# Kernel tuning notes

Measured on AMD Instinct MI355X. Metric: run time of the kernel, lower is better.

The kernel has to match this reference:

```python
import jax, jax.numpy as jnp
import numpy as np

B, L, HID, H, DH = 1, 2048, 1024, 16, 64
KW = 2  # d_conv
EPS = float(np.finfo(np.float32).eps)  # torch RMSNorm eps=None -> dtype eps


def _causal_dw_conv(x, w, b):
    # x: (B, L, D), w: (D, K), b: (D,). Depthwise causal conv, no activation.
    Bs, Ls, D = x.shape
    K = w.shape[1]
    xp = jnp.pad(x, ((0, 0), (K - 1, 0), (0, 0)))
    out = b
    for k in range(K):
        out = out + xp[:, k:k + Ls, :] * w[:, k]
    return out


def setup_inputs() -> dict:
    key = jax.random.key(0)
    ks = jax.random.split(key, 14)
    hidden_states = jax.random.normal(ks[0], (B, L, HID), jnp.float32)
    # masked_fill(attention_mask != 0, -inf): True above diagonal (future masked)
    attention_mask = jnp.triu(jnp.ones((L, L), dtype=bool), 1)[None, None]
    all_dim = 3 * H * DH  # q_size + 2*kv_size with KVH == H
    qkv_w = jax.random.normal(ks[1], (all_dim, HID), jnp.float32) * 0.02
    q_conv_w = jax.random.normal(ks[2], (H * DH, KW), jnp.float32) * 0.5
    q_conv_b = jax.random.normal(ks[3], (H * DH,), jnp.float32) * 0.02
    k_conv_w = jax.random.normal(ks[4], (H * DH, KW), jnp.float32) * 0.5
    k_conv_b = jax.random.normal(ks[5], (H * DH,), jnp.float32) * 0.02
    v_conv_w = jax.random.normal(ks[6], (H * DH, KW), jnp.float32) * 0.5
    v_conv_b = jax.random.normal(ks[7], (H * DH,), jnp.float32) * 0.02
    norm_w = jnp.ones((DH,), jnp.float32)
    A_log = jnp.log(jax.random.uniform(ks[8], (H,), jnp.float32, 1.0, 16.0))
    dt0 = jnp.exp(jax.random.uniform(ks[9], (H,), jnp.float32)
                  * (np.log(0.1) - np.log(0.001)) + np.log(0.001))
    dt0 = jnp.clip(dt0, 1e-4)
    dt_bias = dt0 + jnp.log(-jnp.expm1(-dt0))  # inverse softplus init
    dt_proj_w = jax.random.normal(ks[10], (H, HID), jnp.float32) * 0.02
    dt_proj_b = jnp.zeros((H,), jnp.float32)
    o_w = jax.random.normal(ks[11], (HID, H * DH), jnp.float32) * 0.02
    order_coeff = jnp.ones((1, H, 1, 1), jnp.float32)  # 1/cumprod(arange(1,2))
    return dict(hidden_states=hidden_states, attention_mask=attention_mask,
                qkv_w=qkv_w, q_conv_w=q_conv_w, q_conv_b=q_conv_b,
                k_conv_w=k_conv_w, k_conv_b=k_conv_b, v_conv_w=v_conv_w,
                v_conv_b=v_conv_b, norm_w=norm_w, A_log=A_log, dt_bias=dt_bias,
                dt_proj_w=dt_proj_w, dt_proj_b=dt_proj_b, o_w=o_w,
                order_coeff=order_coeff)


def reference(hidden_states, attention_mask, qkv_w, q_conv_w, q_conv_b,
              k_conv_w, k_conv_b, v_conv_w, v_conv_b, norm_w, A_log, dt_bias,
              dt_proj_w, dt_proj_b, o_w, order_coeff):
    qs = H * DH
    qkv = hidden_states @ qkv_w.T                    # (B, L, 3*H*DH)
    q = _causal_dw_conv(qkv[..., :qs], q_conv_w, q_conv_b)
    k = _causal_dw_conv(qkv[..., qs:2 * qs], k_conv_w, k_conv_b)
    v = _causal_dw_conv(qkv[..., 2 * qs:], v_conv_w, v_conv_b)
    # split heads -> (B, H, L, DH)
    q = q.reshape(B, L, H, DH).transpose(0, 2, 1, 3)
    k = k.reshape(B, L, H, DH).transpose(0, 2, 1, 3)
    v = v.reshape(B, L, H, DH).transpose(0, 2, 1, 3)
    # SSM-style gate: dt (B, L, H)
    dt = jax.nn.softplus(hidden_states @ dt_proj_w.T + dt_proj_b + dt_bias)
    v = v * jnp.swapaxes(dt, 1, 2)[..., None]        # value scaled by dt
    A = -jnp.exp(A_log)[None, None, :] * dt          # (B, L, H)
    A_cumsum = jnp.swapaxes(jnp.cumsum(A, axis=1), 1, 2)  # (B, H, L)
    diff = A_cumsum[:, :, :, None] - A_cumsum[:, :, None, :]  # (B, H, L, L)
    A_mask = jnp.exp(jnp.where(attention_mask, -jnp.inf, diff))
    # order == 1: Taylor series reduces to a single gated linear term
    scores = jnp.einsum('bhld,bhmd->bhlm', q, k) * A_mask * (1.0 / order_coeff)
    out = scores @ v                                  # (B, H, L, DH)
    # RMSNorm over head_dim
    out = out * jax.lax.rsqrt(jnp.mean(out * out, -1, keepdims=True) + EPS) * norm_w
    out = out.transpose(0, 2, 1, 3).reshape(B, L, H * DH)
    return out @ o_w.T
```

## Files before the change

### kernel.cpp

```cpp
#include <hip/hip_runtime.h>
#include <hip/hip_bf16.h>

#define L_SEQ 2048
#define HIDN  1024
#define NH    16
#define DHD   64
#define QKV_P 3200
#define QC_S  2048
#define LP    72

typedef float f4 __attribute__((ext_vector_type(4)));
typedef __bf16 bf16x8 __attribute__((ext_vector_type(8)));
typedef _Float16 half8 __attribute__((ext_vector_type(8)));

union H8 {
  half8 h;
  uint4 u4;
};

__device__ __forceinline__ float b2f(unsigned short u) {
  union { unsigned int i; float f; } c; c.i = ((unsigned int)u) << 16; return c.f;
}
__device__ __forceinline__ unsigned short f2b(float f) {
  union { float f; unsigned int i; } c; c.f = f;
  unsigned int r = c.i + 0x7FFFu + ((c.i >> 16) & 1u);
  return (unsigned short)(r >> 16);
}
__device__ __forceinline__ unsigned short f2h(float f) {
  union { _Float16 h; unsigned short u; } c; c.h = (_Float16)f; return c.u;
}

__global__ __launch_bounds__(256) void prep_kernel(
    const void* hs, const void* qkvw, const void* ow, const void* dtw,
    const void* qw, const void* qb, const void* kw, const void* kb,
    const void* vw, const void* vb, const void* nw, const void* al,
    const void* dtb, const void* dpb, const void* oc,
    unsigned short* __restrict__ hs_b, unsigned short* __restrict__ qkvw_b,
    unsigned short* __restrict__ ow_b,
    float* __restrict__ smallf, int* __restrict__ flag)
{
  __shared__ int cnt;
  if (threadIdx.x == 0) cnt = 0;
  __syncthreads();
  {
    const unsigned short* p = (const unsigned short*)hs;
    int c = 0;
    for (int i = threadIdx.x; i < 8192; i += 256)
      if (((p[i] >> 7) & 0xFFu) >= 140u) c++;
    atomicAdd(&cnt, c);
  }
  __syncthreads();
  const int f = (cnt >= 32) ? 1 : 0;
  if (blockIdx.x == 0 && threadIdx.x == 0) *flag = f;

  const int tid = blockIdx.x * 256 + threadIdx.x;
  const int nth = gridDim.x * 256;
  for (int i = tid; i < 1605632; i += nth) {
    const void* src; unsigned short* dst; int off;
    if (i < 524288)       { src = hs;   dst = hs_b;   off = i; }
    else if (i < 1310720) { src = qkvw; dst = qkvw_b; off = i - 524288; }
    else if (i < 1314816) { src = dtw;  dst = qkvw_b + 3072 * 1024; off = i - 1310720; }
    else if (i < 1343488) {
      *(ushort4*)(qkvw_b + 3088 * 1024 + (i - 1314816) * 4) = (ushort4){0, 0, 0, 0};
      continue;
    }
    else                  { src = ow;   dst = ow_b;   off = i - 1343488; }
    const int e = off * 4;
    if (f) {
      f4 v = *(const f4*)((const float*)src + e);
      ushort4 o;
      o.x = f2b(v[0]); o.y = f2b(v[1]); o.z = f2b(v[2]); o.w = f2b(v[3]);
      *(ushort4*)(dst + e) = o;
    } else {
      *(uint2*)(dst + e) = *(const uint2*)((const unsigned short*)src + e);
    }
  }
  const void* ptrs[11] = {qw, qb, kw, kb, vw, vb, nw, al, dtb, dpb, oc};
  const int sizes[11] = {2048, 1024, 2048, 1024, 2048, 1024, 64, 16, 16, 16, 16};
  int off = 0;
  for (int a = 0; a < 11; ++a) {
    for (int i = tid; i < sizes[a]; i += nth)
      smallf[off + i] = f ? ((const float*)ptrs[a])[i]
                          : b2f(((const unsigned short*)ptrs[a])[i]);
    off += sizes[a];
  }
}

__global__ __launch_bounds__(256) void gemm128(
    const unsigned short* __restrict__ A, const unsigned short* __restrict__ B,
    float* __restrict__ C, int M, int N, int K)
{
  __shared__ __align__(16) unsigned short As[128 * 40];
  __shared__ __align__(16) unsigned short Bs[128 * 40];
  const int t = threadIdx.x;
  const int w = t >> 6, lane = t & 63;
  const int quad = lane >> 4, l16 = lane & 15;
  const int wr = w >> 1, wc = w & 1;
  const int m0 = blockIdx.y * 128, n0 = blockIdx.x * 128;
  const int srow = t >> 1;
  const int scol = (t & 1) * 16;

  f4 acc[4][4];
#pragma unroll
  for (int i = 0; i < 4; ++i)
#pragma unroll
    for (int j = 0; j < 4; ++j) acc[i][j] = (f4){0.f, 0.f, 0.f, 0.f};

  const unsigned short* apg = A + (size_t)(m0 + srow) * K + scol;
  const unsigned short* bpg = B + (size_t)(n0 + srow) * K + scol;
  uint4 a0 = *(const uint4*)apg,       a1 = *(const uint4*)(apg + 8);
  uint4 b0 = *(const uint4*)bpg,       b1 = *(const uint4*)(bpg + 8);

  for (int k0 = 0; k0 < K; k0 += 32) {
    __syncthreads();
    *(uint4*)&As[srow * 40 + scol]     = a0;
    *(uint4*)&As[srow * 40 + scol + 8] = a1;
    *(uint4*)&Bs[srow * 40 + scol]     = b0;
    *(uint4*)&Bs[srow * 40 + scol + 8] = b1;
    __syncthreads();
    if (k0 + 32 < K) {
      a0 = *(const uint4*)(apg + k0 + 32); a1 = *(const uint4*)(apg + k0 + 40);
      b0 = *(const uint4*)(bpg + k0 + 32); b1 = *(const uint4*)(bpg + k0 + 40);
    }
    bf16x8 aF[4], bF[4];
#pragma unroll
    for (int i = 0; i < 4; ++i)
      aF[i] = *(const bf16x8*)&As[(wr * 64 + i * 16 + l16) * 40 + quad * 8];
#pragma unroll
    for (int j = 0; j < 4; ++j)
      bF[j] = *(const bf16x8*)&Bs[(wc * 64 + j * 16 + l16) * 40 + quad * 8];
#pragma unroll
    for (int i = 0; i < 4; ++i)
#pragma unroll
      for (int j = 0; j < 4; ++j)
        acc[i][j] = __builtin_amdgcn_mfma_f32_16x16x32_bf16(aF[i], bF[j], acc[i][j], 0, 0, 0);
  }

#pragma unroll
  for (int i = 0; i < 4; ++i)
#pragma unroll
    for (int j = 0; j < 4; ++j)
#pragma unroll
      for (int r = 0; r < 4; ++r) {
        int m = m0 + wr * 64 + i * 16 + quad * 4 + r;
        int n = n0 + wc * 64 + j * 16 + l16;
        C[(size_t)m * N + n] = acc[i][j][r];
      }
}

template <int MODE>
__global__ __launch_bounds__(256) void gemm_bt(
    const unsigned short* __restrict__ A, const unsigned short* __restrict__ B,
    void* __restrict__ Cv, int M, int N, int K, const int* __restrict__ flag)
{
  __shared__ __align__(16) short As[64 * 40];
  __shared__ __align__(16) short Bs[64 * 40];
  const int t = threadIdx.x;
  const int wave = t >> 6, lane = t & 63;
  const int quad = lane >> 4, l16 = lane & 15;
  const int m0 = blockIdx.y * 64, n0 = blockIdx.x * 64;
  const int srow = t >> 2, scol = (t & 3) * 8;
  f4 acc[4];
#pragma unroll
  for (int i = 0; i < 4; ++i) acc[i] = (f4){0.f, 0.f, 0.f, 0.f};
  const unsigned short* ap = A + (size_t)(m0 + srow) * K + scol;
  const unsigned short* bp = B + (size_t)(n0 + srow) * K + scol;
  for (int k0 = 0; k0 < K; k0 += 32) {
    uint4 av = *(const uint4*)(ap + k0);
    uint4 bv = *(const uint4*)(bp + k0);
    __syncthreads();
    *(uint4*)&As[srow * 40 + scol] = av;
    *(uint4*)&Bs[srow * 40 + scol] = bv;
    __syncthreads();
    bf16x8 af = *(const bf16x8*)&As[(wave * 16 + l16) * 40 + quad * 8];
#pragma unroll
    for (int nt = 0; nt < 4; ++nt) {
      bf16x8 bf = *(const bf16x8*)&Bs[(nt * 16 + l16) * 40 + quad * 8];
      acc[nt] = __builtin_amdgcn_mfma_f32_16x16x32_bf16(af, bf, acc[nt], 0, 0, 0);
    }
  }
  const int outf32 = (MODE == 0) ? 1 : (*flag ? 1 : 0);
#pragma unroll
  for (int nt = 0; nt < 4; ++nt) {
#pragma unroll
    for (int r = 0; r < 4; ++r) {
      int m = m0 + wave * 16 + quad * 4 + r;
      int n = n0 + nt * 16 + l16;
      if (outf32) ((float*)Cv)[(size_t)m * N + n] = acc[nt][r];
      else        ((unsigned short*)Cv)[(size_t)m * N + n] = f2b(acc[nt][r]);
    }
  }
}

__global__ __launch_bounds__(256) void conv_kernel(
    const float* __restrict__ qkvf, const float* __restrict__ smallf,
    unsigned short* __restrict__ qc, unsigned short* __restrict__ vt,
    float* __restrict__ Ac)
{
  if (blockIdx.x < 4096) {
    const int idx = blockIdx.x * 256 + threadIdx.x;
    const int l = idx >> 9;
    const int c = (idx & 511) * 4;
    f4 xc = *(const f4*)&qkvf[(size_t)l * QKV_P + c];
    f4 xp = (f4){0.f, 0.f, 0.f, 0.f};
    if (l > 0) xp = *(const f4*)&qkvf[(size_t)(l - 1) * QKV_P + c];
    const float* w; const float* b; int cb;
    if (c < HIDN) { w = smallf;        b = smallf + 2048; cb = c; }
    else          { w = smallf + 3072; b = smallf + 5120; cb = c - HIDN; }
    f4 o;
#pragma unroll
    for (int j = 0; j < 4; ++j)
      o[j] = b[cb + j] + xp[j] * w[(cb + j) * 2] + xc[j] * w[(cb + j) * 2 + 1];
    ushort4 st;
    st.x = f2h(o[0]); st.y = f2h(o[1]); st.z = f2h(o[2]); st.w = f2h(o[3]);
    *(ushort4*)&qc[(size_t)l * QC_S + c] = st;
  } else if (blockIdx.x < 4608) {
    __shared__ __align__(16) unsigned short Ts[64 * 68];
    const int bv = blockIdx.x - 4096;
    const int h = bv & 15;
    const int lt0 = bv >> 4;
    const int t = threadIdx.x;
    const int srow = t >> 2, cc = t & 3;
    const int l = lt0 * 64 + srow;
    const int cb = h * 64 + cc * 16;
    const float* w = smallf + 6144;
    const float* b = smallf + 8192;
    const float z = qkvf[(size_t)l * QKV_P + 3072 + h]
                  + smallf[9312 + h] + smallf[9296 + h];
    const float dtv = (z > 20.f) ? z : log1pf(expf(z));
    const float* xcp = &qkvf[(size_t)l * QKV_P + 2048 + cb];
    const float* xpp = &qkvf[(size_t)(l - 1) * QKV_P + 2048 + cb];
    unsigned short o16[16];
#pragma unroll
    for (int g = 0; g < 4; ++g) {
      f4 xc = *(const f4*)(xcp + g * 4);
      f4 xp = (f4){0.f, 0.f, 0.f, 0.f};
      if (l > 0) xp = *(const f4*)(xpp + g * 4);
#pragma unroll
      for (int j = 0; j < 4; ++j) {
        const int ch = cb + g * 4 + j;
        float o = b[ch] + xp[j] * w[ch * 2] + xc[j] * w[ch * 2 + 1];
        o16[g * 4 + j] = f2h(o * dtv);
      }
    }
    *(uint4*)&Ts[srow * 68 + cc * 16]     = *(const uint4*)&o16[0];
    *(uint4*)&Ts[srow * 68 + cc * 16 + 8] = *(const uint4*)&o16[8];
    __syncthreads();
    __align__(16) unsigned short o[16];
#pragma unroll
    for (int j = 0; j < 16; ++j) o[j] = Ts[(cc * 16 + j) * 68 + srow];
    unsigned short* op = vt + ((size_t)h * DHD + srow) * L_SEQ + lt0 * 64 + cc * 16;
    *(uint4*)op = *(const uint4*)&o[0];
    *(uint4*)(op + 8) = *(const uint4*)&o[8];
  } else {
    const int h = blockIdx.x - 4608;
    const int lane = threadIdx.x;
    if (lane < 64) {
      const int base = lane * 32;
      const float dpb = smallf[9312 + h], dtb = smallf[9296 + h];
      const float nal = -expf(smallf[9280 + h]);
      float Av[32];
      float run = 0.f;
#pragma unroll
      for (int i = 0; i < 32; ++i) {
        const int l = base + i;
        float z = qkvf[(size_t)l * QKV_P + 3072 + h] + dpb + dtb;
        float dtv = (z > 20.f) ? z : log1pf(expf(z));
        Av[i] = nal * dtv;
        run += Av[i];
      }
      float incl = run;
#pragma unroll
      for (int off = 1; off < 64; off <<= 1) {
        float n = __shfl_up(incl, off);
        if (lane >= off) incl += n;
      }
      float r2 = incl - run;
#pragma unroll
      for (int i = 0; i < 32; ++i) {
        r2 += Av[i];
        Ac[h * L_SEQ + base + i] = r2;
      }
    }
  }
}

__global__ __launch_bounds__(256) void attn_kernel(
    const unsigned short* __restrict__ qc,
    const unsigned short* __restrict__ vt,
    const float* __restrict__ Ac,
    const float* __restrict__ smallf,
    float* __restrict__ po)
{
  const int n  = blockIdx.x;
  const int r_ = n & 7;
  const int hh = (n >> 3) & 1;
  const int k_ = n >> 4;
  const int h  = r_ + 8 * hh;
  const int lt = 31 - (k_ >> 1);
  const int s_ = k_ & 1;
  const int nT = lt + 1;
  const int mS = s_ ? ((nT + 1) >> 1) : 0;
  const int mE = s_ ? nT : ((nT + 1) >> 1);

  const int t  = threadIdx.x;
  const int w    = t >> 6;
  const int lane = t & 63;
  const int l16  = lane & 15;
  const int quad = lane >> 4;
  const int srow = t >> 2;
  const int cc   = t & 3;

  __shared__ __align__(16) unsigned short K_lds[2][64 * LP];
  __shared__ __align__(16) unsigned short V_lds[2][64 * LP];
  __shared__ __align__(16) unsigned short S_lds[64 * LP];

  const int l0 = lt * 64;
  const float rc = 1.0f / smallf[9328 + h];
  const float* Acp = Ac + h * L_SEQ;

  H8 qf0, qf1;
  {
    const unsigned short* qp =
        qc + (size_t)(l0 + w * 16 + l16) * QC_S + h * DHD + quad * 8;
    qf0.u4 = *(const uint4*)qp;
    qf1.u4 = *(const uint4*)(qp + 32);
  }
  float alv[4];
#pragma unroll
  for (int r = 0; r < 4; ++r) alv[r] = Acp[l0 + w * 16 + quad * 4 + r];

  f4 acc[4];
#pragma unroll
  for (int i = 0; i < 4; ++i) acc[i] = (f4){0.f, 0.f, 0.f, 0.f};

  const unsigned short* kgp =
      qc + (size_t)srow * QC_S + HIDN + h * DHD + cc * 16;
  const unsigned short* vgp =
      vt + ((size_t)h * DHD + srow) * L_SEQ + cc * 16;
  const int swo = srow * LP + cc * 16;

  if (mS < mE) {
    uint4 k0v = *(const uint4*)(kgp + (size_t)mS * 64 * QC_S);
    uint4 k1v = *(const uint4*)(kgp + (size_t)mS * 64 * QC_S + 8);
    uint4 v0v = *(const uint4*)(vgp + (size_t)mS * 64);
    uint4 v1v = *(const uint4*)(vgp + (size_t)mS * 64 + 8);
    float amv[4];
#pragma unroll
    for (int nt = 0; nt < 4; ++nt) amv[nt] = Acp[mS * 64 + nt * 16 + l16];

    *(uint4*)&K_lds[0][swo]     = k0v;
    *(uint4*)&K_lds[0][swo + 8] = k1v;
    *(uint4*)&V_lds[0][swo]     = v0v;
    *(uint4*)&V_lds[0][swo + 8] = v1v;
    __syncthreads();

    int cur = 0;
    for (int it = mS; it < mE; ++it) {
      uint4 nk0 = k0v, nk1 = k1v, nv0 = v0v, nv1 = v1v;
      float namv[4];
      const bool more = (it + 1 < mE);
      if (more) {
        const unsigned short* kp = kgp + (size_t)(it + 1) * 64 * QC_S;
        const unsigned short* vp = vgp + (size_t)(it + 1) * 64;
        nk0 = *(const uint4*)kp; nk1 = *(const uint4*)(kp + 8);
        nv0 = *(const uint4*)vp; nv1 = *(const uint4*)(vp + 8);
#pragma unroll
        for (int nt = 0; nt < 4; ++nt)
          namv[nt] = Acp[(it + 1) * 64 + nt * 16 + l16];
      }

      f4 s[4];
#pragma unroll
      for (int i = 0; i < 4; ++i) s[i] = (f4){0.f, 0.f, 0.f, 0.f};
#pragma unroll
      for (int ks = 0; ks < 2; ++ks) {
        H8 qk = ks ? qf1 : qf0;
#pragma unroll
        for (int nt = 0; nt < 4; ++nt) {
          H8 kf;
          kf.u4 = *(const uint4*)&K_lds[cur][(nt * 16 + l16) * LP + ks * 32 + quad * 8];
          s[nt] = __builtin_amdgcn_mfma_f32_16x16x32_f16(qk.h, kf.h, s[nt], 0, 0, 0);
        }
      }
      const int m0 = it * 64;
      if (it == lt) {
#pragma unroll
        for (int nt = 0; nt < 4; ++nt) {
          const int mg = m0 + nt * 16 + l16;
          const float am = amv[nt];
#pragma unroll
          for (int r = 0; r < 4; ++r) {
            const int lg = l0 + w * 16 + quad * 4 + r;
            float val = (mg <= lg) ? s[nt][r] * __expf(alv[r] - am) * rc : 0.0f;
            S_lds[(w * 16 + quad * 4 + r) * LP + nt * 16 + l16] = f2h(val);
          }
        }
      } else {
#pragma unroll
        for (int nt = 0; nt < 4; ++nt) {
          const float am = amv[nt];
#pragma unroll
          for (int r = 0; r < 4; ++r) {
            float val = s[nt][r] * __expf(alv[r] - am) * rc;
            S_lds[(w * 16 + quad * 4 + r) * LP + nt * 16 + l16] = f2h(val);
          }
        }
      }
#pragma unroll
      for (int ks = 0; ks < 2; ++ks) {
        H8 sa;
        sa.u4 = *(const uint4*)&S_lds[(w * 16 + l16) * LP + ks * 32 + quad * 8];
#pragma unroll
        for (int db = 0; db < 4; ++db) {
          H8 vb;
          vb.u4 = *(const uint4*)&V_lds[cur][(db * 16 + l16) * LP + ks * 32 + quad * 8];
          acc[db] = __builtin_amdgcn_mfma_f32_16x16x32_f16(sa.h, vb.h, acc[db], 0, 0, 0);
        }
      }
      if (more) {
        unsigned short* Kl = K_lds[cur ^ 1];
        unsigned short* Vl = V_lds[cur ^ 1];
        *(uint4*)&Kl[swo]     = nk0;
        *(uint4*)&Kl[swo + 8] = nk1;
        *(uint4*)&Vl[swo]     = nv0;
        *(uint4*)&Vl[swo + 8] = nv1;
#pragma unroll
        for (int nt = 0; nt < 4; ++nt) amv[nt] = namv[nt];
        __syncthreads();
        cur ^= 1;
      }
    }
  }

  float* pout = po + (size_t)s_ * (L_SEQ * HIDN);
#pragma unroll
  for (int r = 0; r < 4; ++r) {
    float* op = pout + (size_t)(l0 + w * 16 + quad * 4 + r) * HIDN + h * DHD + l16;
#pragma unroll
    for (int db = 0; db < 4; ++db)
      op[db * 16] = acc[db][r];
  }
}

__global__ __launch_bounds__(256) void reduce_kernel(
    const float* __restrict__ po, const float* __restrict__ smallf,
    unsigned short* __restrict__ attn_out)
{
  const int l = blockIdx.x;
  const int t = threadIdx.x;
  const int col = t * 4;
  const float* p0 = po + (size_t)l * HIDN + col;
  const float* p1 = p0 + (size_t)L_SEQ * HIDN;
  f4 a = *(const f4*)p0;
  f4 b = *(const f4*)p1;
  f4 o = a + b;
  float p = o[0] * o[0] + o[1] * o[1] + o[2] * o[2] + o[3] * o[3];
#pragma unroll
  for (int off = 1; off < 16; off <<= 1) p += __shfl_xor(p, off);
  const float rn = rsqrtf(p * (1.0f / 64.0f) + 1.1920928955078125e-07f);
  const int d0 = col & 63;
  ushort4 st;
  st.x = f2b(o[0] * rn * smallf[9216 + d0]);
  st.y = f2b(o[1] * rn * smallf[9216 + d0 + 1]);
  st.z = f2b(o[2] * rn * smallf[9216 + d0 + 2]);
  st.w = f2b(o[3] * rn * smallf[9216 + d0 + 3]);
  *(ushort4*)&attn_out[(size_t)l * HIDN + col] = st;
}

extern "C" void kernel_launch(void* const* d_in, const int* in_sizes, int n_in,
                              void* d_out, int out_size, void* d_ws, size_t ws_size,
                              hipStream_t stream)
{
  (void)in_sizes; (void)n_in; (void)out_size; (void)ws_size;
  const void* hs        = d_in[0];
  const void* qkv_w     = d_in[2];
  const void* q_conv_w  = d_in[3];
  const void* q_conv_b  = d_in[4];
  const void* k_conv_w  = d_in[5];
  const void* k_conv_b  = d_in[6];
  const void* v_conv_w  = d_in[7];
  const void* v_conv_b  = d_in[8];
  const void* norm_w    = d_in[9];
  const void* A_log     = d_in[10];
  const void* dt_bias   = d_in[11];
  const void* dt_proj_w = d_in[12];
  const void* dt_proj_b = d_in[13];
  const void* o_w       = d_in[14];
  const void* ordc      = d_in[15];

  char* ws = (char*)d_ws;
  int* flag             = (int*)ws;
  unsigned short* hs_b  = (unsigned short*)(ws + 256);
  unsigned short* qkvw_b= (unsigned short*)(ws + 4194560);
  unsigned short* ow_b  = (unsigned short*)(ws + 10748160);
  float* smallf         = (float*)(ws + 12845312);
  float* qkvf           = (float*)(ws + 12882688);
  unsigned short* qc_h  = (unsigned short*)(ws + 39097088);
  float* Acum           = (float*)(ws + 47616768);
  unsigned short* attnb = (unsigned short*)(ws + 47747840);
  unsigned short* vt_h  = (unsigned short*)(ws + 51942144);
  float* po             = (float*)(ws + 56136448);

  prep_kernel<<<1024, 256, 0, stream>>>(
      hs, qkv_w, o_w, dt_proj_w,
      q_conv_w, q_conv_b, k_conv_w, k_conv_b, v_conv_w, v_conv_b,
      norm_w, A_log, dt_bias, dt_proj_b, ordc,
      hs_b, qkvw_b, ow_b, smallf, flag);

  gemm128<<<dim3(QKV_P / 128, L_SEQ / 128), 256, 0, stream>>>(
      hs_b, qkvw_b, qkvf, L_SEQ, QKV_P, HIDN);
  conv_kernel<<<4096 + 512 + 16, 256, 0, stream>>>(qkvf, smallf, qc_h, vt_h, Acum);
  attn_kernel<<<1024, 256, 0, stream>>>(qc_h, vt_h, Acum, smallf, po);
  reduce_kernel<<<L_SEQ, 256, 0, stream>>>(po, smallf, attnb);
  gemm_bt<1><<<dim3(HIDN / 64, L_SEQ / 64), 256, 0, stream>>>(
      attnb, ow_b, d_out, L_SEQ, HIDN, HIDN, flag);
}
```

Baseline: 220.7 us.

## Load GEMM tiles directly into LDS and raise wave priority around MFMA blocks

The bf16 GEMM now stages A/B tiles with global_load_lds (direct global-to-LDS DMA) into an unpadded 32-wide layout, replacing the register prefetch and the ds_write of the staging data. The cost it targets is the VGPR round trip and the extra LDS store instructions. In exchange, the loads are no longer overlapped with the previous tile's MFMAs, and the unpadded stride may cause LDS bank conflicts on fragment reads. Separately, the attention kernel wraps its two MFMA loops in s_setprio to favour matrix issue across waves.

```diff
diff --git a/kernel.cpp b/kernel.cpp
--- a/kernel.cpp
+++ b/kernel.cpp
@@ -90,15 +90,15 @@
     const unsigned short* __restrict__ A, const unsigned short* __restrict__ B,
     float* __restrict__ C, int M, int N, int K)
 {
-  __shared__ __align__(16) unsigned short As[128 * 40];
-  __shared__ __align__(16) unsigned short Bs[128 * 40];
+  __shared__ __align__(16) unsigned short As[128 * 32];
+  __shared__ __align__(16) unsigned short Bs[128 * 32];
   const int t = threadIdx.x;
-  const int w = t >> 6, lane = t & 63;
+  const int wv = t >> 6, lane = t & 63;
   const int quad = lane >> 4, l16 = lane & 15;
-  const int wr = w >> 1, wc = w & 1;
+  const int wr = wv >> 1, wc = wv & 1;
   const int m0 = blockIdx.y * 128, n0 = blockIdx.x * 128;
-  const int srow = t >> 1;
-  const int scol = (t & 1) * 16;
+  const int crow = lane >> 2;
+  const int ccol = (lane & 3) * 8;
 
   f4 acc[4][4];
 #pragma unroll
@@ -106,29 +106,34 @@
 #pragma unroll
     for (int j = 0; j < 4; ++j) acc[i][j] = (f4){0.f, 0.f, 0.f, 0.f};
 
-  const unsigned short* apg = A + (size_t)(m0 + srow) * K + scol;
-  const unsigned short* bpg = B + (size_t)(n0 + srow) * K + scol;
-  uint4 a0 = *(const uint4*)apg,       a1 = *(const uint4*)(apg + 8);
-  uint4 b0 = *(const uint4*)bpg,       b1 = *(const uint4*)(bpg + 8);
+  const int c0 = wv * 2, c1 = wv * 2 + 1;
+  const unsigned short* ga0 = A + (size_t)(m0 + c0 * 16 + crow) * K + ccol;
+  const unsigned short* ga1 = A + (size_t)(m0 + c1 * 16 + crow) * K + ccol;
+  const unsigned short* gb0 = B + (size_t)(n0 + c0 * 16 + crow) * K + ccol;
+  const unsigned short* gb1 = B + (size_t)(n0 + c1 * 16 + crow) * K + ccol;
+  unsigned short* la0 = &As[c0 * 512];
+  unsigned short* la1 = &As[c1 * 512];
+  unsigned short* lb0 = &Bs[c0 * 512];
+  unsigned short* lb1 = &Bs[c1 * 512];
 
   for (int k0 = 0; k0 < K; k0 += 32) {
     __syncthreads();
-    *(uint4*)&As[srow * 40 + scol]     = a0;
-    *(uint4*)&As[srow * 40 + scol + 8] = a1;
-    *(uint4*)&Bs[srow * 40 + scol]     = b0;
-    *(uint4*)&Bs[srow * 40 + scol + 8] = b1;
+    __builtin_amdgcn_global_load_lds((const unsigned int*)(ga0 + k0),
+                                     (unsigned int*)la0, 16, 0, 0);
+    __builtin_amdgcn_global_load_lds((const unsigned int*)(ga1 + k0),
+                                     (unsigned int*)la1, 16, 0, 0);
+    __builtin_amdgcn_global_load_lds((const unsigned int*)(gb0 + k0),
+                                     (unsigned int*)lb0, 16, 0, 0);
+    __builtin_amdgcn_global_load_lds((const unsigned int*)(gb1 + k0),
+                                     (unsigned int*)lb1, 16, 0, 0);
     __syncthreads();
-    if (k0 + 32 < K) {
-      a0 = *(const uint4*)(apg + k0 + 32); a1 = *(const uint4*)(apg + k0 + 40);
-      b0 = *(const uint4*)(bpg + k0 + 32); b1 = *(const uint4*)(bpg + k0 + 40);
-    }
     bf16x8 aF[4], bF[4];
 #pragma unroll
     for (int i = 0; i < 4; ++i)
-      aF[i] = *(const bf16x8*)&As[(wr * 64 + i * 16 + l16) * 40 + quad * 8];
+      aF[i] = *(const bf16x8*)&As[(wr * 64 + i * 16 + l16) * 32 + quad * 8];
 #pragma unroll
     for (int j = 0; j < 4; ++j)
-      bF[j] = *(const bf16x8*)&Bs[(wc * 64 + j * 16 + l16) * 40 + quad * 8];
+      bF[j] = *(const bf16x8*)&Bs[(wc * 64 + j * 16 + l16) * 32 + quad * 8];
 #pragma unroll
     for (int i = 0; i < 4; ++i)
 #pragma unroll
@@ -373,6 +378,7 @@
       f4 s[4];
 #pragma unroll
       for (int i = 0; i < 4; ++i) s[i] = (f4){0.f, 0.f, 0.f, 0.f};
+      __builtin_amdgcn_s_setprio(1);
 #pragma unroll
       for (int ks = 0; ks < 2; ++ks) {
         H8 qk = ks ? qf1 : qf0;
@@ -383,6 +389,7 @@
           s[nt] = __builtin_amdgcn_mfma_f32_16x16x32_f16(qk.h, kf.h, s[nt], 0, 0, 0);
         }
       }
+      __builtin_amdgcn_s_setprio(0);
       const int m0 = it * 64;
       if (it == lt) {
 #pragma unroll
@@ -407,6 +414,7 @@
           }
         }
       }
+      __builtin_amdgcn_s_setprio(1);
 #pragma unroll
       for (int ks = 0; ks < 2; ++ks) {
         H8 sa;
@@ -418,6 +426,7 @@
           acc[db] = __builtin_amdgcn_mfma_f32_16x16x32_f16(sa.h, vb.h, acc[db], 0, 0, 0);
         }
       }
+      __builtin_amdgcn_s_setprio(0);
       if (more) {
         unsigned short* Kl = K_lds[cur ^ 1];
         unsigned short* Vl = V_lds[cur ^ 1];
```

Result: no change. 221.1 us (+0.2%).

## Fuse input dtype conversion into GEMM loads and drop the prep kernel

Applied to the files above, without the earlier changes.

Removes the separate prep kernel that converted inputs and weights to bf16 and gathered the small parameters. The QKV GEMM and the output GEMM now read the raw inputs and convert fp32 to bf16 on the fly while loading tiles. The other kernels read the small parameters straight from the inputs through a flag-dependent loader. This saves one launch and a full read/write pass over the weights, at the cost of reading fp32 (twice the bytes) inside the GEMM loops and repeating conversions per tile. It also adds s_setprio around the MFMA sections in the attention kernel.

```diff
diff --git a/kernel.cpp b/kernel.cpp
--- a/kernel.cpp
+++ b/kernel.cpp
@@ -29,21 +29,34 @@
 __device__ __forceinline__ unsigned short f2h(float f) {
   union { _Float16 h; unsigned short u; } c; c.h = (_Float16)f; return c.u;
 }
-
-__global__ __launch_bounds__(256) void prep_kernel(
-    const void* hs, const void* qkvw, const void* ow, const void* dtw,
-    const void* qw, const void* qb, const void* kw, const void* kb,
-    const void* vw, const void* vb, const void* nw, const void* al,
-    const void* dtb, const void* dpb, const void* oc,
-    unsigned short* __restrict__ hs_b, unsigned short* __restrict__ qkvw_b,
-    unsigned short* __restrict__ ow_b,
-    float* __restrict__ smallf, int* __restrict__ flag)
+__device__ __forceinline__ float ldp(const void* p, int i, int f) {
+  return f ? ((const float*)p)[i] : b2f(((const unsigned short*)p)[i]);
+}
+__device__ __forceinline__ uint4 ld8cvt(const void* base, size_t eoff, int f) {
+  if (f) {
+    const float* p = (const float*)base + eoff;
+    f4 v0 = *(const f4*)p, v1 = *(const f4*)(p + 4);
+    uint4 r;
+    r.x = (unsigned)f2b(v0[0]) | ((unsigned)f2b(v0[1]) << 16);
+    r.y = (unsigned)f2b(v0[2]) | ((unsigned)f2b(v0[3]) << 16);
+    r.z = (unsigned)f2b(v1[0]) | ((unsigned)f2b(v1[1]) << 16);
+    r.w = (unsigned)f2b(v1[2]) | ((unsigned)f2b(v1[3]) << 16);
+    return r;
+  }
+  return *(const uint4*)((const unsigned short*)base + eoff);
+}
+
+__global__ __launch_bounds__(256) void gemm128(
+    const void* __restrict__ Araw,
+    const void* __restrict__ Braw,
+    const void* __restrict__ Draw,
+    float* __restrict__ C, int* __restrict__ flagOut)
 {
   __shared__ int cnt;
   if (threadIdx.x == 0) cnt = 0;
   __syncthreads();
   {
-    const unsigned short* p = (const unsigned short*)hs;
+    const unsigned short* p = (const unsigned short*)Araw;
     int c = 0;
     for (int i = threadIdx.x; i < 8192; i += 256)
       if (((p[i] >> 7) & 0xFFu) >= 140u) c++;
@@ -51,45 +64,8 @@
   }
   __syncthreads();
   const int f = (cnt >= 32) ? 1 : 0;
-  if (blockIdx.x == 0 && threadIdx.x == 0) *flag = f;
-
-  const int tid = blockIdx.x * 256 + threadIdx.x;
-  const int nth = gridDim.x * 256;
-  for (int i = tid; i < 1605632; i += nth) {
-    const void* src; unsigned short* dst; int off;
-    if (i < 524288)       { src = hs;   dst = hs_b;   off = i; }
-    else if (i < 1310720) { src = qkvw; dst = qkvw_b; off = i - 524288; }
-    else if (i < 1314816) { src = dtw;  dst = qkvw_b + 3072 * 1024; off = i - 1310720; }
-    else if (i < 1343488) {
-      *(ushort4*)(qkvw_b + 3088 * 1024 + (i - 1314816) * 4) = (ushort4){0, 0, 0, 0};
-      continue;
-    }
-    else                  { src = ow;   dst = ow_b;   off = i - 1343488; }
-    const int e = off * 4;
-    if (f) {
-      f4 v = *(const f4*)((const float*)src + e);
-      ushort4 o;
-      o.x = f2b(v[0]); o.y = f2b(v[1]); o.z = f2b(v[2]); o.w = f2b(v[3]);
-      *(ushort4*)(dst + e) = o;
-    } else {
-      *(uint2*)(dst + e) = *(const uint2*)((const unsigned short*)src + e);
-    }
-  }
-  const void* ptrs[11] = {qw, qb, kw, kb, vw, vb, nw, al, dtb, dpb, oc};
-  const int sizes[11] = {2048, 1024, 2048, 1024, 2048, 1024, 64, 16, 16, 16, 16};
-  int off = 0;
-  for (int a = 0; a < 11; ++a) {
-    for (int i = tid; i < sizes[a]; i += nth)
-      smallf[off + i] = f ? ((const float*)ptrs[a])[i]
-                          : b2f(((const unsigned short*)ptrs[a])[i]);
-    off += sizes[a];
-  }
-}
-
-__global__ __launch_bounds__(256) void gemm128(
-    const unsigned short* __restrict__ A, const unsigned short* __restrict__ B,
-    float* __restrict__ C, int M, int N, int K)
-{
+  if (blockIdx.x == 0 && blockIdx.y == 0 && threadIdx.x == 0) *flagOut = f;
+
   __shared__ __align__(16) unsigned short As[128 * 40];
   __shared__ __align__(16) unsigned short Bs[128 * 40];
   const int t = threadIdx.x;
@@ -106,21 +82,26 @@
 #pragma unroll
     for (int j = 0; j < 4; ++j) acc[i][j] = (f4){0.f, 0.f, 0.f, 0.f};
 
-  const unsigned short* apg = A + (size_t)(m0 + srow) * K + scol;
-  const unsigned short* bpg = B + (size_t)(n0 + srow) * K + scol;
-  uint4 a0 = *(const uint4*)apg,       a1 = *(const uint4*)(apg + 8);
-  uint4 b0 = *(const uint4*)bpg,       b1 = *(const uint4*)(bpg + 8);
-
-  for (int k0 = 0; k0 < K; k0 += 32) {
+  const size_t aoff = (size_t)(m0 + srow) * 1024 + scol;
+  const int grow = n0 + srow;
+  const void* bsrc; size_t boff;
+  if (grow < 3072)      { bsrc = Braw; boff = (size_t)grow * 1024 + scol; }
+  else if (grow < 3088) { bsrc = Draw; boff = (size_t)(grow - 3072) * 1024 + scol; }
+  else                  { bsrc = Draw; boff = (size_t)scol; }
+
+  uint4 a0 = ld8cvt(Araw, aoff, f),     a1 = ld8cvt(Araw, aoff + 8, f);
+  uint4 b0 = ld8cvt(bsrc, boff, f),     b1 = ld8cvt(bsrc, boff + 8, f);
+
+  for (int k0 = 0; k0 < 1024; k0 += 32) {
     __syncthreads();
     *(uint4*)&As[srow * 40 + scol]     = a0;
     *(uint4*)&As[srow * 40 + scol + 8] = a1;
     *(uint4*)&Bs[srow * 40 + scol]     = b0;
     *(uint4*)&Bs[srow * 40 + scol + 8] = b1;
     __syncthreads();
-    if (k0 + 32 < K) {
-      a0 = *(const uint4*)(apg + k0 + 32); a1 = *(const uint4*)(apg + k0 + 40);
-      b0 = *(const uint4*)(bpg + k0 + 32); b1 = *(const uint4*)(bpg + k0 + 40);
+    if (k0 + 32 < 1024) {
+      a0 = ld8cvt(Araw, aoff + k0 + 32, f); a1 = ld8cvt(Araw, aoff + k0 + 40, f);
+      b0 = ld8cvt(bsrc, boff + k0 + 32, f); b1 = ld8cvt(bsrc, boff + k0 + 40, f);
     }
     bf16x8 aF[4], bF[4];
 #pragma unroll
@@ -144,17 +125,18 @@
       for (int r = 0; r < 4; ++r) {
         int m = m0 + wr * 64 + i * 16 + quad * 4 + r;
         int n = n0 + wc * 64 + j * 16 + l16;
-        C[(size_t)m * N + n] = acc[i][j][r];
-      }
-}
-
-template <int MODE>
-__global__ __launch_bounds__(256) void gemm_bt(
-    const unsigned short* __restrict__ A, const unsigned short* __restrict__ B,
-    void* __restrict__ Cv, int M, int N, int K, const int* __restrict__ flag)
+        C[(size_t)m * QKV_P + n] = acc[i][j][r];
+      }
+}
+
+__global__ __launch_bounds__(256) void gemm_out(
+    const unsigned short* __restrict__ A,
+    const void* __restrict__ Braw,
+    void* __restrict__ Cv, const int* __restrict__ flag)
 {
   __shared__ __align__(16) short As[64 * 40];
   __shared__ __align__(16) short Bs[64 * 40];
+  const int f = *flag;
   const int t = threadIdx.x;
   const int wave = t >> 6, lane = t & 63;
   const int quad = lane >> 4, l16 = lane & 15;
@@ -163,11 +145,11 @@
   f4 acc[4];
 #pragma unroll
   for (int i = 0; i < 4; ++i) acc[i] = (f4){0.f, 0.f, 0.f, 0.f};
-  const unsigned short* ap = A + (size_t)(m0 + srow) * K + scol;
-  const unsigned short* bp = B + (size_t)(n0 + srow) * K + scol;
-  for (int k0 = 0; k0 < K; k0 += 32) {
+  const unsigned short* ap = A + (size_t)(m0 + srow) * HIDN + scol;
+  const size_t boff = (size_t)(n0 + srow) * HIDN + scol;
+  for (int k0 = 0; k0 < HIDN; k0 += 32) {
     uint4 av = *(const uint4*)(ap + k0);
-    uint4 bv = *(const uint4*)(bp + k0);
+    uint4 bv = ld8cvt(Braw, boff + k0, f);
     __syncthreads();
     *(uint4*)&As[srow * 40 + scol] = av;
     *(uint4*)&Bs[srow * 40 + scol] = bv;
@@ -179,24 +161,27 @@
       acc[nt] = __builtin_amdgcn_mfma_f32_16x16x32_bf16(af, bf, acc[nt], 0, 0, 0);
     }
   }
-  const int outf32 = (MODE == 0) ? 1 : (*flag ? 1 : 0);
 #pragma unroll
   for (int nt = 0; nt < 4; ++nt) {
 #pragma unroll
     for (int r = 0; r < 4; ++r) {
       int m = m0 + wave * 16 + quad * 4 + r;
       int n = n0 + nt * 16 + l16;
-      if (outf32) ((float*)Cv)[(size_t)m * N + n] = acc[nt][r];
-      else        ((unsigned short*)Cv)[(size_t)m * N + n] = f2b(acc[nt][r]);
+      if (f) ((float*)Cv)[(size_t)m * HIDN + n] = acc[nt][r];
+      else   ((unsigned short*)Cv)[(size_t)m * HIDN + n] = f2b(acc[nt][r]);
     }
   }
 }
 
 __global__ __launch_bounds__(256) void conv_kernel(
-    const float* __restrict__ qkvf, const float* __restrict__ smallf,
+    const float* __restrict__ qkvf,
+    const void* qw, const void* qb, const void* kw, const void* kb,
+    const void* vw, const void* vb, const void* dtb, const void* dpb,
+    const void* al, const int* __restrict__ flag,
     unsigned short* __restrict__ qc, unsigned short* __restrict__ vt,
     float* __restrict__ Ac)
 {
+  const int f = *flag;
   if (blockIdx.x < 4096) {
     const int idx = blockIdx.x * 256 + threadIdx.x;
     const int l = idx >> 9;
@@ -204,13 +189,14 @@
     f4 xc = *(const f4*)&qkvf[(size_t)l * QKV_P + c];
     f4 xp = (f4){0.f, 0.f, 0.f, 0.f};
     if (l > 0) xp = *(const f4*)&qkvf[(size_t)(l - 1) * QKV_P + c];
-    const float* w; const float* b; int cb;
-    if (c < HIDN) { w = smallf;        b = smallf + 2048; cb = c; }
-    else          { w = smallf + 3072; b = smallf + 5120; cb = c - HIDN; }
+    const void* w; const void* b; int cb;
+    if (c < HIDN) { w = qw; b = qb; cb = c; }
+    else          { w = kw; b = kb; cb = c - HIDN; }
     f4 o;
 #pragma unroll
     for (int j = 0; j < 4; ++j)
-      o[j] = b[cb + j] + xp[j] * w[(cb + j) * 2] + xc[j] * w[(cb + j) * 2 + 1];
+      o[j] = ldp(b, cb + j, f) + xp[j] * ldp(w, (cb + j) * 2, f)
+           + xc[j] * ldp(w, (cb + j) * 2 + 1, f);
     ushort4 st;
     st.x = f2h(o[0]); st.y = f2h(o[1]); st.z = f2h(o[2]); st.w = f2h(o[3]);
     *(ushort4*)&qc[(size_t)l * QC_S + c] = st;
@@ -223,10 +209,8 @@
     const int srow = t >> 2, cc = t & 3;
     const int l = lt0 * 64 + srow;
     const int cb = h * 64 + cc * 16;
-    const float* w = smallf + 6144;
-    const float* b = smallf + 8192;
     const float z = qkvf[(size_t)l * QKV_P + 3072 + h]
-                  + smallf[9312 + h] + smallf[9296 + h];
+                  + ldp(dpb, h, f) + ldp(dtb, h, f);
     const float dtv = (z > 20.f) ? z : log1pf(expf(z));
     const float* xcp = &qkvf[(size_t)l * QKV_P + 2048 + cb];
     const float* xpp = &qkvf[(size_t)(l - 1) * QKV_P + 2048 + cb];
@@ -239,7 +223,8 @@
 #pragma unroll
       for (int j = 0; j < 4; ++j) {
         const int ch = cb + g * 4 + j;
-        float o = b[ch] + xp[j] * w[ch * 2] + xc[j] * w[ch * 2 + 1];
+        float o = ldp(vb, ch, f) + xp[j] * ldp(vw, ch * 2, f)
+                + xc[j] * ldp(vw, ch * 2 + 1, f);
         o16[g * 4 + j] = f2h(o * dtv);
       }
     }
@@ -257,14 +242,14 @@
     const int lane = threadIdx.x;
     if (lane < 64) {
       const int base = lane * 32;
-      const float dpb = smallf[9312 + h], dtb = smallf[9296 + h];
-      const float nal = -expf(smallf[9280 + h]);
+      const float dpbv = ldp(dpb, h, f), dtbv = ldp(dtb, h, f);
+      const float nal = -expf(ldp(al, h, f));
       float Av[32];
       float run = 0.f;
 #pragma unroll
       for (int i = 0; i < 32; ++i) {
         const int l = base + i;
-        float z = qkvf[(size_t)l * QKV_P + 3072 + h] + dpb + dtb;
+        float z = qkvf[(size_t)l * QKV_P + 3072 + h] + dpbv + dtbv;
         float dtv = (z > 20.f) ? z : log1pf(expf(z));
         Av[i] = nal * dtv;
         run += Av[i];
@@ -289,7 +274,7 @@
     const unsigned short* __restrict__ qc,
     const unsigned short* __restrict__ vt,
     const float* __restrict__ Ac,
-    const float* __restrict__ smallf,
+    const void* __restrict__ ordc, const int* __restrict__ flag,
     float* __restrict__ po)
 {
   const int n  = blockIdx.x;
@@ -316,7 +301,7 @@
   __shared__ __align__(16) unsigned short S_lds[64 * LP];
 
   const int l0 = lt * 64;
-  const float rc = 1.0f / smallf[9328 + h];
+  const float rc = 1.0f / ldp(ordc, h, *flag);
   const float* Acp = Ac + h * L_SEQ;
 
   H8 qf0, qf1;
@@ -373,6 +358,7 @@
       f4 s[4];
 #pragma unroll
       for (int i = 0; i < 4; ++i) s[i] = (f4){0.f, 0.f, 0.f, 0.f};
+      __builtin_amdgcn_s_setprio(1);
 #pragma unroll
       for (int ks = 0; ks < 2; ++ks) {
         H8 qk = ks ? qf1 : qf0;
@@ -383,6 +369,7 @@
           s[nt] = __builtin_amdgcn_mfma_f32_16x16x32_f16(qk.h, kf.h, s[nt], 0, 0, 0);
         }
       }
+      __builtin_amdgcn_s_setprio(0);
       const int m0 = it * 64;
       if (it == lt) {
 #pragma unroll
@@ -407,6 +394,7 @@
           }
         }
       }
+      __builtin_amdgcn_s_setprio(1);
 #pragma unroll
       for (int ks = 0; ks < 2; ++ks) {
         H8 sa;
@@ -418,6 +406,7 @@
           acc[db] = __builtin_amdgcn_mfma_f32_16x16x32_f16(sa.h, vb.h, acc[db], 0, 0, 0);
         }
       }
+      __builtin_amdgcn_s_setprio(0);
       if (more) {
         unsigned short* Kl = K_lds[cur ^ 1];
         unsigned short* Vl = V_lds[cur ^ 1];
@@ -444,9 +433,10 @@
 }
 
 __global__ __launch_bounds__(256) void reduce_kernel(
-    const float* __restrict__ po, const float* __restrict__ smallf,
-    unsigned short* __restrict__ attn_out)
+    const float* __restrict__ po, const void* __restrict__ nw,
+    const int* __restrict__ flag, unsigned short* __restrict__ attn_out)
 {
+  const int f = *flag;
   const int l = blockIdx.x;
   const int t = threadIdx.x;
   const int col = t * 4;
@@ -461,10 +451,10 @@
   const float rn = rsqrtf(p * (1.0f / 64.0f) + 1.1920928955078125e-07f);
   const int d0 = col & 63;
   ushort4 st;
-  st.x = f2b(o[0] * rn * smallf[9216 + d0]);
-  st.y = f2b(o[1] * rn * smallf[9216 + d0 + 1]);
-  st.z = f2b(o[2] * rn * smallf[9216 + d0 + 2]);
-  st.w = f2b(o[3] * rn * smallf[9216 + d0 + 3]);
+  st.x = f2b(o[0] * rn * ldp(nw, d0, f));
+  st.y = f2b(o[1] * rn * ldp(nw, d0 + 1, f));
+  st.z = f2b(o[2] * rn * ldp(nw, d0 + 2, f));
+  st.w = f2b(o[3] * rn * ldp(nw, d0 + 3, f));
   *(ushort4*)&attn_out[(size_t)l * HIDN + col] = st;
 }
 
@@ -491,28 +481,20 @@
 
   char* ws = (char*)d_ws;
   int* flag             = (int*)ws;
-  unsigned short* hs_b  = (unsigned short*)(ws + 256);
-  unsigned short* qkvw_b= (unsigned short*)(ws + 4194560);
-  unsigned short* ow_b  = (unsigned short*)(ws + 10748160);
-  float* smallf         = (float*)(ws + 12845312);
-  float* qkvf           = (float*)(ws + 12882688);
-  unsigned short* qc_h  = (unsigned short*)(ws + 39097088);
-  float* Acum           = (float*)(ws + 47616768);
-  unsigned short* attnb = (unsigned short*)(ws + 47747840);
-  unsigned short* vt_h  = (unsigned short*)(ws + 51942144);
-  float* po             = (float*)(ws + 56136448);
-
-  prep_kernel<<<1024, 256, 0, stream>>>(
-      hs, qkv_w, o_w, dt_proj_w,
-      q_conv_w, q_conv_b, k_conv_w, k_conv_b, v_conv_w, v_conv_b,
-      norm_w, A_log, dt_bias, dt_proj_b, ordc,
-      hs_b, qkvw_b, ow_b, smallf, flag);
+  float* qkvf           = (float*)(ws + 256);
+  unsigned short* qc_h  = (unsigned short*)(ws + 26214656);
+  unsigned short* vt_h  = (unsigned short*)(ws + 34603264);
+  float* Acum           = (float*)(ws + 38797568);
+  unsigned short* attnb = (unsigned short*)(ws + 38928640);
+  float* po             = (float*)(ws + 43122944);
 
   gemm128<<<dim3(QKV_P / 128, L_SEQ / 128), 256, 0, stream>>>(
-      hs_b, qkvw_b, qkvf, L_SEQ, QKV_P, HIDN);
-  conv_kernel<<<4096 + 512 + 16, 256, 0, stream>>>(qkvf, smallf, qc_h, vt_h, Acum);
-  attn_kernel<<<1024, 256, 0, stream>>>(qc_h, vt_h, Acum, smallf, po);
-  reduce_kernel<<<L_SEQ, 256, 0, stream>>>(po, smallf, attnb);
-  gemm_bt<1><<<dim3(HIDN / 64, L_SEQ / 64), 256, 0, stream>>>(
-      attnb, ow_b, d_out, L_SEQ, HIDN, HIDN, flag);
-}
+      hs, qkv_w, dt_proj_w, qkvf, flag);
+  conv_kernel<<<4096 + 512 + 16, 256, 0, stream>>>(
+      qkvf, q_conv_w, q_conv_b, k_conv_w, k_conv_b, v_conv_w, v_conv_b,
+      dt_bias, dt_proj_b, A_log, flag, qc_h, vt_h, Acum);
+  attn_kernel<<<1024, 256, 0, stream>>>(qc_h, vt_h, Acum, ordc, flag, po);
+  reduce_kernel<<<L_SEQ, 256, 0, stream>>>(po, norm_w, flag, attnb);
+  gemm_out<<<dim3(HIDN / 64, L_SEQ / 64), 256, 0, stream>>>(
+      attnb, o_w, d_out, flag);
+}
```

After: 267.7 us. +21.3%, slower.
